# Performance work log

Hardware: AMD Instinct MI355X
Metric: run time of the kernel (lower is better)

## Reference

```python
import jax, jax.numpy as jnp
import numpy as np

T, N, E = 64, 10000, 160000
NIN, NHID, NOUT = 64, 128, 64

def _xavier(key, shape):
    # xavier_normal_ for Linear/GCNConv lin weights of shape [out, in]
    std = jnp.sqrt(2.0 / (shape[0] + shape[1])).astype(jnp.float32)
    return std * jax.random.normal(key, shape, dtype=jnp.float32)

def setup_inputs() -> dict:
    key = jax.random.key(0)
    ks = jax.random.split(key, 12)
    x = jax.random.normal(ks[0], (T, N, NIN), dtype=jnp.float32)
    src = jax.random.randint(ks[1], (E,), 0, N)
    dst = jax.random.randint(ks[2], (E,), 0, N)
    edge_index = jnp.stack([src, dst])  # [2, E], PyG convention src->dst
    m_in = dst   # receiver index per edge (one-hot row of incidence matrix)
    m_out = src  # sender index per edge
    b = 0.1 * jnp.ones((NHID,), jnp.float32)
    return {
        "x": x, "edge_index": edge_index, "m_in": m_in, "m_out": m_out,
        "Wi": _xavier(ks[3], (NHID, NIN + NHID)), "bi": b,
        "Wf": _xavier(ks[4], (NHID, NIN + NHID)), "bf": b,
        "Wo": _xavier(ks[5], (NHID, NIN + NHID)), "bo": b,
        "Wg": _xavier(ks[6], (NHID, NIN + NHID)), "bg": b,
        "W1": _xavier(ks[7], (NHID, 2 * NHID)), "b1": b,
        "Wc": _xavier(ks[8], (NOUT, NHID)), "bc": 0.1 * jnp.ones((NOUT,), jnp.float32),
    }

def reference(x, edge_index, m_in, m_out, Wi, bi, Wf, bf, Wo, bo, Wg, bg, W1, b1, Wc, bc):
    n = x.shape[1]
    src, dst = edge_index[0], edge_index[1]
    loop = jnp.arange(n)
    s = jnp.concatenate([src, loop])  # self-loops appended (GCNConv default)
    d = jnp.concatenate([dst, loop])
    deg = jax.ops.segment_sum(jnp.ones_like(d, x.dtype), d, num_segments=n)
    dinv = jnp.where(deg > 0, deg, 1.0) ** -0.5  # deg>=1 with self-loops
    norm = (dinv[s] * dinv[d])[:, None]

    def gcn(z, W, b):
        zw = z @ W.T                    # [n, out]
        return jax.ops.segment_sum(zw[s] * norm, d, num_segments=n) + b

    def step(carry, xt):
        h, c = carry
        comb = jnp.concatenate([xt, h], axis=-1)  # [n, n_in+n_hid]
        i = jax.nn.sigmoid(gcn(comb, Wi, bi))
        f = jax.nn.sigmoid(gcn(comb, Wf, bf))
        o = jax.nn.sigmoid(gcn(comb, Wo, bo))
        g = jnp.tanh(gcn(comb, Wg, bg))
        c = f * c + i * g
        h = o * jnp.tanh(c)
        return (h, c), None

    h0 = jnp.zeros((n, NHID), x.dtype)
    (h, _), _ = jax.lax.scan(step, (h0, h0), x)

    # node2edge: concat receiver and sender hidden states  [E, 2*n_hid]
    e = jnp.concatenate([h[m_in], h[m_out]], axis=-1)
    e = jax.nn.relu(e @ W1.T + b1)  # dropout p=0.0 -> identity
    # edge2node: scatter-sum edge features to receiver nodes
    nodes = jax.ops.segment_sum(e, m_in, num_segments=n)
    return gcn(nodes, Wc, bc)
```

## Files before the change

### kernel.cpp

```cpp
#include <hip/hip_runtime.h>
#include <math.h>

#define NIN 64
#define NHID 128
#define NOUT 64

typedef __bf16 bf16x8 __attribute__((ext_vector_type(8)));
typedef float  floatx4 __attribute__((ext_vector_type(4)));

__device__ __forceinline__ float fsig(float x){
  return __fdividef(1.0f, 1.0f + __expf(-x));
}
__device__ __forceinline__ float ftanh(float x){
  return 1.0f - 2.0f*__fdividef(1.0f, 1.0f + __expf(2.0f*x));
}
__device__ __forceinline__ float b2f_lo(unsigned p){ unsigned b = p<<16; return __uint_as_float(b); }
__device__ __forceinline__ float b2f_hi(unsigned p){ unsigned b = p & 0xffff0000u; return __uint_as_float(b); }
__device__ __forceinline__ unsigned f2pk(float lo, float hi){
  __bf16 a=(__bf16)lo, b=(__bf16)hi;
  unsigned short ua, ub;
  __builtin_memcpy(&ua,&a,2); __builtin_memcpy(&ub,&b,2);
  return (unsigned)ua | ((unsigned)ub<<16);
}

__global__ void k_deg_init(int* __restrict__ deg, int n){
  int v = blockIdx.x*256 + threadIdx.x;
  if(v<n) deg[v] = 1;
}
__global__ void k_deg_count(const int* __restrict__ dst, int E, int* __restrict__ deg){
  int e = blockIdx.x*256 + threadIdx.x;
  if(e<E) atomicAdd(&deg[dst[e]], 1);
}
__global__ void k_dinv(const int* __restrict__ deg, float* __restrict__ dinv, int n){
  int v = blockIdx.x*256 + threadIdx.x;
  if(v<n) dinv[v] = rsqrtf((float)deg[v]);
}
__global__ __launch_bounds__(1024) void k_scan(const int* __restrict__ deg,
    int* __restrict__ row_ptr, int* __restrict__ fill, int n){
  __shared__ int lds[1024];
  const int t = threadIdx.x;
  const int per = (n + 1023)/1024;
  int a = t*per, b = a+per; if(b>n) b=n;
  int local=0;
  for(int v=a; v<b; ++v) local += deg[v]-1;
  lds[t]=local;
  __syncthreads();
  for(int off=1; off<1024; off<<=1){
    int x=(t>=off)? lds[t-off]:0;
    __syncthreads();
    lds[t]+=x;
    __syncthreads();
  }
  int run = lds[t]-local;
  for(int v=a; v<b; ++v){
    row_ptr[v]=run; fill[v]=run;
    run += deg[v]-1;
  }
  if(t==1023) row_ptr[n]=lds[1023];
}
__global__ void k_fill(const int* __restrict__ src, const int* __restrict__ dst, int E,
                       int* __restrict__ fill, int* __restrict__ ecol){
  int e = blockIdx.x*256 + threadIdx.x;
  if(e<E){
    int d = dst[e];
    int pos = atomicAdd(&fill[d], 1);
    ecol[pos] = src[e];
  }
}

__global__ void k_prep_wb(const float* __restrict__ Wi, const float* __restrict__ Wf,
                          const float* __restrict__ Wo, const float* __restrict__ Wg,
                          __bf16* __restrict__ Wb){
  int idx = blockIdx.x*256 + threadIdx.x;
  if(idx >= 32*6*64*8) return;
  int jj = idx & 7;
  int L  = (idx >> 3) & 63;
  int t  = idx >> 9;
  int kt = t - (t/6)*6, CT = t/6;
  int colj = CT*16 + (L & 15);
  int k    = kt*32 + ((L >> 4) << 3) + jj;
  int gate = colj >> 7, jg = colj & 127;
  const float* W = (gate==0)? Wi : (gate==1)? Wf : (gate==2)? Wo : Wg;
  Wb[idx] = (__bf16)W[jg*192 + k];
}
__global__ void k_prep_w1(const float* __restrict__ W1, float* __restrict__ W1t){
  int idx = blockIdx.x*256 + threadIdx.x;
  if(idx >= 128*256) return;
  int k = idx >> 8, j = idx & 255;
  W1t[idx] = (j<128)? W1[j*256+k] : W1[(j-128)*256+128+k];
}
__global__ void k_prep_wc(const float* __restrict__ Wc, float* __restrict__ Wct){
  int idx = blockIdx.x*256 + threadIdx.x;
  if(idx >= 128*64) return;
  int k = idx/64, j = idx%64;
  Wct[idx] = Wc[j*128+k];
}

__global__ void k_init(unsigned* __restrict__ hpA, unsigned* __restrict__ hpB,
                       unsigned* __restrict__ cbufp, __bf16* __restrict__ xs,
                       int NP, int T){
  int i = blockIdx.x*256 + threadIdx.x;
  if(i < (NP+1)*64){ hpA[i]=0u; hpB[i]=0u; }
  if(i < NP*64) cbufp[i]=0u;
  if(i < T*64){ int t=i>>6, f=i&63; xs[((size_t)t*(NP+1) + NP)*64 + f] = (__bf16)0.f; }
}

__global__ void k_xscale(const float* __restrict__ x, const float* __restrict__ dinv,
                         __bf16* __restrict__ xs, int n, int NP){
  int i = blockIdx.x*256 + threadIdx.x;
  if(i >= n*8) return;
  int t = blockIdx.y;
  float dv = dinv[i>>3];
  const float4* xp = (const float4*)(x + (size_t)t*(size_t)n*64) + (size_t)i*2;
  float4 a = xp[0], b = xp[1];
  bf16x8 o;
  o[0]=(__bf16)(a.x*dv); o[1]=(__bf16)(a.y*dv); o[2]=(__bf16)(a.z*dv); o[3]=(__bf16)(a.w*dv);
  o[4]=(__bf16)(b.x*dv); o[5]=(__bf16)(b.y*dv); o[6]=(__bf16)(b.z*dv); o[7]=(__bf16)(b.w*dv);
  *(bf16x8*)(xs + ((size_t)t*(NP+1))*64 + (size_t)i*8) = o;
}

__global__ __launch_bounds__(512,5) void k_step(
    const __bf16* __restrict__ xst,
    const unsigned* __restrict__ hp_prev,
    unsigned* __restrict__ hp_cur,
    unsigned* __restrict__ cbufp,
    float* __restrict__ hbuf,
    const int* __restrict__ row_ptr, const int* __restrict__ ecol,
    const float* __restrict__ dinv, const __bf16* __restrict__ Wb,
    const float* __restrict__ bi, const float* __restrict__ bf_,
    const float* __restrict__ bo, const float* __restrict__ bg,
    int n, int NP, int last)
{
  __shared__ __align__(16) __bf16 s_a[6*544];
  __shared__ int   s_col[1024];
  __shared__ int   s_deg[16];
  __shared__ int   s_beg[16];
  __shared__ float s_dv[16];
  const int tid=threadIdx.x, wv=tid>>6, l=tid&63;
  const int l15=l&15, quad=l>>4;
  const int v0=blockIdx.x*16;

  if(tid<16){
    int v=v0+tid;
    int beg=(v<n)? row_ptr[v]:0, end=(v<n)? row_ptr[v+1]:0;
    s_beg[tid]=beg; s_deg[tid]=end-beg;
    s_dv[tid]=(v<n)? dinv[v]:0.f;
  }
  __syncthreads();
  for(int idx=tid; idx<1024; idx+=512){
    int m=idx>>6, kk=idx&63;
    s_col[idx]=(kk<s_deg[m])? ecol[s_beg[m]+kk] : NP;
  }
  __syncthreads();

  float ax[2], alo[2], ahi[2];
  int K;
  {
    int d0=s_deg[2*wv], d1=s_deg[2*wv+1];
    d0=d0>64?64:d0; d1=d1>64?64:d1;
    K=d0>d1?d0:d1;
  }
  #pragma unroll
  for(int i=0;i<2;++i){
    int v=v0+2*wv+i;
    ax[i]=(float)xst[(size_t)v*64+l];
    unsigned p=hp_prev[(size_t)v*64+l];
    alo[i]=b2f_lo(p); ahi[i]=b2f_hi(p);
  }
  const int* cr=&s_col[(2*wv)*64];
  #pragma unroll 4
  for(int kk=0;kk<K;++kk){
    int u0=cr[kk], u1=cr[64+kk];
    float    x0=(float)xst[(size_t)u0*64+l];
    unsigned p0=hp_prev[(size_t)u0*64+l];
    float    x1=(float)xst[(size_t)u1*64+l];
    unsigned p1=hp_prev[(size_t)u1*64+l];
    ax[0]+=x0; alo[0]+=b2f_lo(p0); ahi[0]+=b2f_hi(p0);
    ax[1]+=x1; alo[1]+=b2f_lo(p1); ahi[1]+=b2f_hi(p1);
  }
  #pragma unroll
  for(int i=0;i<2;++i){
    int m=2*wv+i, d=s_deg[m];
    if(d>64){
      for(int e2=s_beg[m]+64;e2<s_beg[m]+d;++e2){
        int u=ecol[e2];
        ax[i]+=(float)xst[(size_t)u*64+l];
        unsigned p=hp_prev[(size_t)u*64+l];
        alo[i]+=b2f_lo(p); ahi[i]+=b2f_hi(p);
      }
    }
  }
  {
    int kt0=l>>5, q0=(l>>3)&3, j0=l&7;
    int L2=2*l, kt1=2+(L2>>5), q1=(L2>>3)&3, j1=L2&7;
    #pragma unroll
    for(int i=0;i<2;++i){
      int m=2*wv+i; float dv=s_dv[m];
      s_a[kt0*544+q0*136+m*8+j0]=(__bf16)(dv*ax[i]);
      *(unsigned*)&s_a[kt1*544+q1*136+m*8+j1]=f2pk(dv*alo[i],dv*ahi[i]);
    }
  }
  __syncthreads();

  bf16x8 af[6];
  #pragma unroll
  for(int kt=0;kt<6;++kt)
    af[kt]=*(bf16x8*)&s_a[kt*544+quad*136+l15*8];
  const int jg=16*wv+l15;
  floatx4 acc[4];
  {
    #pragma unroll
    for(int g=0;g<4;++g){
      const float* bsel = (g==0)? bi : (g==1)? bf_ : (g==2)? bo : bg;
      float b=bsel[jg];
      floatx4 a={b,b,b,b};
      const __bf16* bp=Wb + (size_t)((8*g+wv)*6)*512 + (size_t)l*8;
      #pragma unroll
      for(int kt=0;kt<6;++kt)
        a=__builtin_amdgcn_mfma_f32_16x16x32_bf16(af[kt],*(const bf16x8*)(bp+kt*512),a,0,0,0);
      acc[g]=a;
    }
  }

  #pragma unroll
  for(int r=0;r<4;++r){
    int m=quad*4+r, v=v0+m;
    float I=fsig (acc[0][r]);
    float F=fsig (acc[1][r]);
    float O=fsig (acc[2][r]);
    float G=ftanh(acc[3][r]);
    size_t cw=(size_t)v*64+(jg>>1);
    unsigned cold=cbufp[cw];
    float cprev=(l15&1)? b2f_hi(cold) : b2f_lo(cold);
    float cn=F*cprev+I*G;
    float cn2=__shfl_xor(cn,1,64);
    float hn=O*ftanh(cn);
    float hs=s_dv[m]*hn;
    float hs2=__shfl_xor(hs,1,64);
    if((l15&1)==0){
      cbufp[cw]=f2pk(cn,cn2);
      hp_cur[(size_t)v*64+(jg>>1)]=f2pk(hs,hs2);
    }
    if(last) hbuf[(size_t)v*128+jg]=hn;
  }
}

__global__ __launch_bounds__(256) void k_head1(const float* __restrict__ h,
    const float* __restrict__ W1t, float* __restrict__ Hio, int n){
  __shared__ float s_h[16][NHID];
  int v0 = blockIdx.x*16;
  for(int i=threadIdx.x; i<16*NHID; i+=256){
    int m = i/NHID, k = i - m*NHID;
    int v = v0 + m;
    s_h[m][k] = (v<n)? h[(size_t)v*NHID + k] : 0.0f;
  }
  __syncthreads();
  int j = threadIdx.x;
  float acc[16];
  #pragma unroll
  for(int m=0;m<16;++m) acc[m]=0.f;
  for(int k=0;k<NHID;++k){
    float w = W1t[k*256 + j];
    #pragma unroll
    for(int m=0;m<16;++m) acc[m] = fmaf(w, s_h[m][k], acc[m]);
  }
  for(int m=0;m<16;++m){
    int v = v0 + m;
    if(v >= n) break;
    Hio[(size_t)v*256 + j] = acc[m];
  }
}
__global__ __launch_bounds__(256) void k_e2n(const float* __restrict__ Hio,
    const int* __restrict__ row_ptr, const int* __restrict__ col,
    const float* __restrict__ b1, float* __restrict__ nodes, int n){
  int wv = threadIdx.x >> 6, lane = threadIdx.x & 63;
  int v = blockIdx.x*4 + wv;
  if(v >= n) return;
  float base0 = Hio[(size_t)v*256 + lane]      + b1[lane];
  float base1 = Hio[(size_t)v*256 + 64 + lane] + b1[64+lane];
  float a0=0.f, a1=0.f;
  int beg=row_ptr[v], end=row_ptr[v+1];
  int e=beg;
  for(; e+1<end; e+=2){
    int u0 = col[e], u1 = col[e+1];
    float p0 = Hio[(size_t)u0*256 + 128 + lane];
    float q0 = Hio[(size_t)u0*256 + 192 + lane];
    float p1 = Hio[(size_t)u1*256 + 128 + lane];
    float q1 = Hio[(size_t)u1*256 + 192 + lane];
    a0 += fmaxf(base0 + p0, 0.0f) + fmaxf(base0 + p1, 0.0f);
    a1 += fmaxf(base1 + q0, 0.0f) + fmaxf(base1 + q1, 0.0f);
  }
  if(e<end){
    int u = col[e];
    a0 += fmaxf(base0 + Hio[(size_t)u*256 + 128 + lane], 0.0f);
    a1 += fmaxf(base1 + Hio[(size_t)u*256 + 192 + lane], 0.0f);
  }
  nodes[(size_t)v*NHID + lane]      = a0;
  nodes[(size_t)v*NHID + 64 + lane] = a1;
}
__global__ __launch_bounds__(64) void k_head2(const float* __restrict__ nodes,
    const float* __restrict__ Wct, float* __restrict__ tmp, int n){
  __shared__ float s_n[16][NHID];
  int v0 = blockIdx.x*16;
  for(int i=threadIdx.x; i<16*NHID; i+=64){
    int m = i/NHID, k = i - m*NHID;
    int v = v0 + m;
    s_n[m][k] = (v<n)? nodes[(size_t)v*NHID + k] : 0.0f;
  }
  __syncthreads();
  int j = threadIdx.x;
  float acc[16];
  #pragma unroll
  for(int m=0;m<16;++m) acc[m]=0.f;
  for(int k=0;k<NHID;++k){
    float w = Wct[k*64 + j];
    #pragma unroll
    for(int m=0;m<16;++m) acc[m] = fmaf(w, s_n[m][k], acc[m]);
  }
  for(int m=0;m<16;++m){
    int v = v0 + m;
    if(v >= n) break;
    tmp[(size_t)v*64 + j] = acc[m];
  }
}
__global__ __launch_bounds__(256) void k_final(const float* __restrict__ tmp,
    const int* __restrict__ row_ptr, const int* __restrict__ col,
    const float* __restrict__ dinv, const float* __restrict__ bc,
    float* __restrict__ out, int n){
  int wv = threadIdx.x >> 6, lane = threadIdx.x & 63;
  int v = blockIdx.x*4 + wv;
  if(v >= n) return;
  float dv = dinv[v];
  float acc = dv*dv*tmp[(size_t)v*64 + lane];
  int beg=row_ptr[v], end=row_ptr[v+1];
  int e=beg;
  for(; e+1<end; e+=2){
    int u0 = col[e], u1 = col[e+1];
    float d0 = dinv[u0], d1 = dinv[u1];
    float t0 = tmp[(size_t)u0*64 + lane];
    float t1 = tmp[(size_t)u1*64 + lane];
    acc = fmaf(dv*d0, t0, acc);
    acc = fmaf(dv*d1, t1, acc);
  }
  if(e<end){
    int u = col[e];
    acc = fmaf(dv*dinv[u], tmp[(size_t)u*64 + lane], acc);
  }
  out[(size_t)v*64 + lane] = acc + bc[lane];
}

extern "C" void kernel_launch(void* const* d_in, const int* in_sizes, int n_in,
                              void* d_out, int out_size, void* d_ws, size_t ws_size,
                              hipStream_t stream) {
  (void)n_in; (void)ws_size;
  const float* x  = (const float*)d_in[0];
  const int*   ei = (const int*)d_in[1];
  const float* Wi = (const float*)d_in[4];  const float* bi  = (const float*)d_in[5];
  const float* Wf = (const float*)d_in[6];  const float* bf_ = (const float*)d_in[7];
  const float* Wo = (const float*)d_in[8];  const float* bo  = (const float*)d_in[9];
  const float* Wg = (const float*)d_in[10]; const float* bg  = (const float*)d_in[11];
  const float* W1 = (const float*)d_in[12]; const float* b1  = (const float*)d_in[13];
  const float* Wc = (const float*)d_in[14]; const float* bc  = (const float*)d_in[15];
  float* out = (float*)d_out;

  const int E = in_sizes[2];
  const int n = out_size / NOUT;
  const int T = in_sizes[0] / (n * NIN);
  const int ntiles = (n + 15)/16;
  const int NP = ntiles*16;
  const int* srcl = ei;
  const int* dstl = ei + E;

  char* p = (char*)d_ws;
  auto alloc = [&](size_t bytes){ char* r = p; p += ((bytes + 255)/256)*256; return r; };
  int*      deg     = (int*)     alloc((size_t)n*4);
  float*    dinv    = (float*)   alloc((size_t)n*4);
  int*      row_ptr = (int*)     alloc((size_t)(n+1)*4);
  int*      fill    = (int*)     alloc((size_t)n*4);
  int*      ecol    = (int*)     alloc((size_t)E*4);
  __bf16*   Wb      = (__bf16*)  alloc((size_t)32*6*64*8*2);
  float*    W1t     = (float*)   alloc((size_t)128*256*4);
  float*    Wct     = (float*)   alloc((size_t)128*64*4);
  __bf16*   xs      = (__bf16*)  alloc((size_t)T*(NP+1)*64*2);
  unsigned* hpA     = (unsigned*)alloc((size_t)(NP+1)*64*4);
  unsigned* hpB     = (unsigned*)alloc((size_t)(NP+1)*64*4);
  unsigned* cbufp   = (unsigned*)alloc((size_t)NP*64*4);
  float*    hbuf    = (float*)   alloc((size_t)NP*128*4);
  float*    Hio     = (float*)   alloc((size_t)NP*256*4);
  float*    nodes   = (float*)   alloc((size_t)n*NHID*4);
  float*    tmp     = (float*)   alloc((size_t)NP*64*4);

  int gn = (n+255)/256;
  int gE = (E+255)/256;

  k_deg_init <<<gn, 256, 0, stream>>>(deg, n);
  k_deg_count<<<gE, 256, 0, stream>>>(dstl, E, deg);
  k_dinv     <<<gn, 256, 0, stream>>>(deg, dinv, n);
  k_scan     <<<1, 1024, 0, stream>>>(deg, row_ptr, fill, n);
  k_fill     <<<gE, 256, 0, stream>>>(srcl, dstl, E, fill, ecol);

  k_prep_wb<<<(32*6*64*8+255)/256, 256, 0, stream>>>(Wi, Wf, Wo, Wg, Wb);
  k_prep_w1<<<(128*256+255)/256, 256, 0, stream>>>(W1, W1t);
  k_prep_wc<<<(128*64+255)/256, 256, 0, stream>>>(Wc, Wct);

  k_init<<<(((NP+1)*64)+255)/256, 256, 0, stream>>>(hpA, hpB, cbufp, xs, NP, T);
  k_xscale<<<dim3((n*8+255)/256, T), 256, 0, stream>>>(x, dinv, xs, n, NP);

  for(int t=0; t<T; ++t){
    const __bf16* xst = xs + (size_t)t*(size_t)(NP+1)*64;
    const unsigned* hp = (t & 1)? hpB : hpA;
    unsigned*       hc = (t & 1)? hpA : hpB;
    k_step<<<ntiles, 512, 0, stream>>>(xst, hp, hc, cbufp, hbuf, row_ptr, ecol, dinv,
                                       Wb, bi, bf_, bo, bg, n, NP, (t==T-1)?1:0);
  }

  k_head1<<<ntiles, 256, 0, stream>>>(hbuf, W1t, Hio, n);
  k_e2n  <<<(n+3)/4, 256, 0, stream>>>(Hio, row_ptr, ecol, b1, nodes, n);
  k_head2<<<(n+15)/16, 64, 0, stream>>>(nodes, Wct, tmp, n);
  k_final<<<(n+3)/4, 256, 0, stream>>>(tmp, row_ptr, ecol, dinv, bc, out, n);
}
```

Baseline: 1.536 ms.

## Sort nodes by in-degree so step tiles have balanced neighbor counts

Builds a degree-sorted node permutation with a histogram, a prefix scan and a scatter, then has each step tile process 16 nodes of similar degree instead of consecutive node ids. The gather loop runs to the maximum degree of a node pair, so grouping nodes of equal degree removes padded iterations and load imbalance across waves. In exchange, reads and writes of the self row, cell state and hidden state become scattered rather than contiguous, and four small preprocessing kernels are added.

Result: slower. 1.609 ms (+4.7%).

```diff
diff --git a/kernel.cpp b/kernel.cpp
--- a/kernel.cpp
+++ b/kernel.cpp
@@ -65,6 +65,43 @@
     int d = dst[e];
     int pos = atomicAdd(&fill[d], 1);
     ecol[pos] = src[e];
+  }
+}
+
+__global__ void k_hzero(int* __restrict__ hist){
+  int i = blockIdx.x*256 + threadIdx.x;
+  if(i<1024) hist[i]=0;
+}
+__global__ void k_hist(const int* __restrict__ deg, int* __restrict__ hist, int n){
+  int v = blockIdx.x*256 + threadIdx.x;
+  if(v<n){
+    int d=deg[v]; if(d>1023)d=1023;
+    atomicAdd(&hist[d],1);
+  }
+}
+__global__ __launch_bounds__(1024) void k_binoff(const int* __restrict__ hist,
+    int* __restrict__ binfill, int n){
+  __shared__ int lds[1024];
+  int t=threadIdx.x;
+  lds[t]=hist[t];
+  __syncthreads();
+  for(int off=1;off<1024;off<<=1){
+    int x=(t>=off)? lds[t-off]:0;
+    __syncthreads();
+    lds[t]+=x;
+    __syncthreads();
+  }
+  binfill[t] = n - lds[t];
+}
+__global__ void k_scatter(const int* __restrict__ deg, int* __restrict__ binfill,
+    int* __restrict__ perm, int n, int NP){
+  int v = blockIdx.x*256 + threadIdx.x;
+  if(v<n){
+    int d=deg[v]; if(d>1023)d=1023;
+    int pos=atomicAdd(&binfill[d],1);
+    perm[pos]=v;
+  } else if(v<NP){
+    perm[v]=n;
   }
 }
 
@@ -126,13 +163,15 @@
     unsigned* __restrict__ cbufp,
     float* __restrict__ hbuf,
     const int* __restrict__ row_ptr, const int* __restrict__ ecol,
-    const float* __restrict__ dinv, const __bf16* __restrict__ Wb,
+    const float* __restrict__ dinv, const int* __restrict__ perm,
+    const __bf16* __restrict__ Wb,
     const float* __restrict__ bi, const float* __restrict__ bf_,
     const float* __restrict__ bo, const float* __restrict__ bg,
     int n, int NP, int last)
 {
   __shared__ __align__(16) __bf16 s_a[6*544];
   __shared__ int   s_col[1024];
+  __shared__ int   s_pv[16];
   __shared__ int   s_deg[16];
   __shared__ int   s_beg[16];
   __shared__ float s_dv[16];
@@ -141,10 +180,13 @@
   const int v0=blockIdx.x*16;
 
   if(tid<16){
-    int v=v0+tid;
-    int beg=(v<n)? row_ptr[v]:0, end=(v<n)? row_ptr[v+1]:0;
+    int idx=v0+tid;
+    int pv=(idx<n)? perm[idx] : n;
+    s_pv[tid]=pv;
+    bool val=(pv<n);
+    int beg=val? row_ptr[pv]:0, end=val? row_ptr[pv+1]:0;
     s_beg[tid]=beg; s_deg[tid]=end-beg;
-    s_dv[tid]=(v<n)? dinv[v]:0.f;
+    s_dv[tid]=val? dinv[pv]:0.f;
   }
   __syncthreads();
   for(int idx=tid; idx<1024; idx+=512){
@@ -162,9 +204,10 @@
   }
   #pragma unroll
   for(int i=0;i<2;++i){
-    int v=v0+2*wv+i;
-    ax[i]=(float)xst[(size_t)v*64+l];
-    unsigned p=hp_prev[(size_t)v*64+l];
+    int pv=s_pv[2*wv+i];
+    int row=(pv<n)? pv : NP;
+    ax[i]=(float)xst[(size_t)row*64+l];
+    unsigned p=hp_prev[(size_t)row*64+l];
     alo[i]=b2f_lo(p); ahi[i]=b2f_hi(p);
   }
   const int* cr=&s_col[(2*wv)*64];
@@ -224,24 +267,26 @@
 
   #pragma unroll
   for(int r=0;r<4;++r){
-    int m=quad*4+r, v=v0+m;
+    int m=quad*4+r;
+    int v=s_pv[m];
+    bool val=(v<n);
     float I=fsig (acc[0][r]);
     float F=fsig (acc[1][r]);
     float O=fsig (acc[2][r]);
     float G=ftanh(acc[3][r]);
-    size_t cw=(size_t)v*64+(jg>>1);
-    unsigned cold=cbufp[cw];
+    size_t cw= val? ((size_t)v*64+(jg>>1)) : 0;
+    unsigned cold= val? cbufp[cw] : 0u;
     float cprev=(l15&1)? b2f_hi(cold) : b2f_lo(cold);
     float cn=F*cprev+I*G;
     float cn2=__shfl_xor(cn,1,64);
     float hn=O*ftanh(cn);
     float hs=s_dv[m]*hn;
     float hs2=__shfl_xor(hs,1,64);
-    if((l15&1)==0){
+    if(val && (l15&1)==0){
       cbufp[cw]=f2pk(cn,cn2);
       hp_cur[(size_t)v*64+(jg>>1)]=f2pk(hs,hs2);
     }
-    if(last) hbuf[(size_t)v*128+jg]=hn;
+    if(val && last) hbuf[(size_t)v*128+jg]=hn;
   }
 }
 
@@ -378,6 +423,9 @@
   int*      row_ptr = (int*)     alloc((size_t)(n+1)*4);
   int*      fill    = (int*)     alloc((size_t)n*4);
   int*      ecol    = (int*)     alloc((size_t)E*4);
+  int*      hist    = (int*)     alloc((size_t)1024*4);
+  int*      binfill = (int*)     alloc((size_t)1024*4);
+  int*      perm    = (int*)     alloc((size_t)NP*4);
   __bf16*   Wb      = (__bf16*)  alloc((size_t)32*6*64*8*2);
   float*    W1t     = (float*)   alloc((size_t)128*256*4);
   float*    Wct     = (float*)   alloc((size_t)128*64*4);
@@ -399,6 +447,11 @@
   k_scan     <<<1, 1024, 0, stream>>>(deg, row_ptr, fill, n);
   k_fill     <<<gE, 256, 0, stream>>>(srcl, dstl, E, fill, ecol);
 
+  k_hzero   <<<4, 256, 0, stream>>>(hist);
+  k_hist    <<<gn, 256, 0, stream>>>(deg, hist, n);
+  k_binoff  <<<1, 1024, 0, stream>>>(hist, binfill, n);
+  k_scatter <<<(NP+255)/256, 256, 0, stream>>>(deg, binfill, perm, n, NP);
+
   k_prep_wb<<<(32*6*64*8+255)/256, 256, 0, stream>>>(Wi, Wf, Wo, Wg, Wb);
   k_prep_w1<<<(128*256+255)/256, 256, 0, stream>>>(W1, W1t);
   k_prep_wc<<<(128*64+255)/256, 256, 0, stream>>>(Wc, Wct);
@@ -411,7 +464,7 @@
     const unsigned* hp = (t & 1)? hpB : hpA;
     unsigned*       hc = (t & 1)? hpA : hpB;
     k_step<<<ntiles, 512, 0, stream>>>(xst, hp, hc, cbufp, hbuf, row_ptr, ecol, dinv,
-                                       Wb, bi, bf_, bo, bg, n, NP, (t==T-1)?1:0);
+                                       perm, Wb, bi, bf_, bo, bg, n, NP, (t==T-1)?1:0);
   }
 
   k_head1<<<ntiles, 256, 0, stream>>>(hbuf, W1t, Hio, n);
```
